# Kernel optimization log

Measured on AMD Instinct MI355X. Metric: run time of the kernel, lower is better.

## Reference

```python
import jax, jax.numpy as jnp
import numpy as np

D_MODEL = 512
D_FF = 2048
D_K = 64
N_HEADS = 8
LN_EPS = 1e-5


def layer_norm(x, gamma, beta):
    mu = jnp.mean(x, axis=-1, keepdims=True)
    var = jnp.mean(jnp.square(x - mu), axis=-1, keepdims=True)
    return (x - mu) * jax.lax.rsqrt(var + LN_EPS) * gamma + beta


def setup_inputs() -> dict:
    key = jax.random.key(0)
    ks = jax.random.split(key, 8)
    B, S = 16, 1024
    s_in = 1.0 / np.sqrt(D_MODEL)
    s_ff = 1.0 / np.sqrt(D_FF)
    return {
        "x": jax.random.normal(ks[0], (B, S, D_MODEL), jnp.float32),
        # shared QKV projection (the module uses ONE linear for Q, K and V)
        "w_qkv": jax.random.uniform(ks[1], (D_MODEL, D_MODEL), jnp.float32, -s_in, s_in),
        "b_qkv": jnp.zeros((D_MODEL,), jnp.float32),
        "w_out": jax.random.uniform(ks[2], (D_MODEL, D_MODEL), jnp.float32, -s_in, s_in),
        "b_out": jnp.zeros((D_MODEL,), jnp.float32),
        "w1": jax.random.uniform(ks[3], (D_FF, D_MODEL), jnp.float32, -s_in, s_in),
        "b1": jnp.zeros((D_FF,), jnp.float32),
        "w2": jax.random.uniform(ks[4], (D_MODEL, D_FF), jnp.float32, -s_ff, s_ff),
        "b2": jnp.zeros((D_MODEL,), jnp.float32),
        "g1": jnp.ones((D_MODEL,), jnp.float32),
        "be1": jnp.zeros((D_MODEL,), jnp.float32),
        "g2": jnp.ones((D_MODEL,), jnp.float32),
        "be2": jnp.zeros((D_MODEL,), jnp.float32),
    }


def reference(x, w_qkv, b_qkv, w_out, b_out, w1, b1, w2, b2, g1, be1, g2, be2):
    B, S, _ = x.shape
    # --- MultiHeadAttention (shared linear for Q/K/V, dropout = identity) ---
    qkv = x @ w_qkv.T + b_qkv                       # [B,S,D]
    h = qkv.reshape(B, S, N_HEADS, D_K)             # Q = K = V
    scores = jnp.einsum("bqhd,bkhd->bhqk", h, h) / np.sqrt(D_K)
    probs = jax.nn.softmax(scores, axis=-1)
    ctx = jnp.einsum("bhqk,bkhd->bqhd", probs, h).reshape(B, S, D_MODEL)
    attn = ctx @ w_out.T + b_out
    # --- dual-LayerNorm residual #1: x = norm1(x) + norm1(attn) ---
    x = layer_norm(x, g1, be1) + layer_norm(attn, g1, be1)
    # --- FFN ---
    ffn = jax.nn.relu(x @ w1.T + b1) @ w2.T + b2
    # --- residual #2: x = x + norm2(ffn) ---
    return x + layer_norm(ffn, g2, be2)
```

## Files before the change

### kernel.cpp

```cpp
#include <hip/hip_runtime.h>
#include <hip/hip_bf16.h>
#include <stdint.h>


using bf16 = __bf16;
typedef __attribute__((ext_vector_type(2))) __bf16 bf16x2;
typedef __attribute__((ext_vector_type(4))) __bf16 bf16x4;
typedef __attribute__((ext_vector_type(8))) __bf16 bf16x8;
typedef __attribute__((ext_vector_type(4))) float floatx4;
typedef __attribute__((ext_vector_type(16))) float f32x16;

#define AS1 __attribute__((address_space(1)))
#define AS3 __attribute__((address_space(3)))

#define L2E 1.44269504088896340736f

constexpr int BN_ = 16, SQ_ = 1024, DM_ = 512, DFF_ = 2048, NH_ = 8, DK_ = 64;
constexpr int ROWS_ = BN_ * SQ_;

__global__ __launch_bounds__(256) void f2b_kernel(const float* __restrict__ in,
                                                  bf16* __restrict__ out, int n8) {
  int i = blockIdx.x * 256 + threadIdx.x;
  if (i >= n8) return;
  float4 a = ((const float4*)in)[2 * i];
  float4 b = ((const float4*)in)[2 * i + 1];
  bf16x8 o;
  o[0] = (bf16)a.x; o[1] = (bf16)a.y; o[2] = (bf16)a.z; o[3] = (bf16)a.w;
  o[4] = (bf16)b.x; o[5] = (bf16)b.y; o[6] = (bf16)b.z; o[7] = (bf16)b.w;
  ((bf16x8*)out)[i] = o;
}

template <int RELU>
__global__ __launch_bounds__(256) void gemm_bt(const bf16* __restrict__ A,
                                               const bf16* __restrict__ B,
                                               const float* __restrict__ bias,
                                               bf16* __restrict__ C,
                                               int M, int N, int K) {
  __shared__ char glds[32768];
  const int tid = threadIdx.x;
  const int lane = tid & 63;
  const int wv = tid >> 6;
  const int wr = wv >> 1, wc = wv & 1;
  const int r15 = lane & 15, g = lane >> 4;
  const int tileN = blockIdx.x * 128;
  const int tileM = blockIdx.y * 128;

  floatx4 acc[4][4] = {};

  uint32_t dstoff[2];
  const bf16* srcA[2];
  const bf16* srcB[2];
#pragma unroll
  for (int is = 0; is < 2; ++is) {
    const int base = wv * 2048 + is * 1024;
    const int ob = base + lane * 16;
    const int row = ob >> 6;
    const int pslot = (ob >> 4) & 3;
    const int sslot = pslot ^ ((row >> 1) & 3);
    dstoff[is] = base;
    srcA[is] = A + (size_t)(tileM + row) * K + sslot * 8;
    srcB[is] = B + (size_t)(tileN + row) * K + sslot * 8;
  }

#define GSTAGE(buf, kt)                                                         \
  {                                                                             \
    _Pragma("unroll")                                                           \
    for (int is = 0; is < 2; ++is) {                                            \
      __builtin_amdgcn_global_load_lds(                                         \
          (AS1 uint32_t*)(srcA[is] + (kt) * 32),                                \
          (AS3 uint32_t*)((AS3 char*)glds + (buf) * 8192 + dstoff[is]), 16, 0, 0); \
      __builtin_amdgcn_global_load_lds(                                         \
          (AS1 uint32_t*)(srcB[is] + (kt) * 32),                                \
          (AS3 uint32_t*)((AS3 char*)glds + 16384 + (buf) * 8192 + dstoff[is]), \
          16, 0, 0);                                                            \
    }                                                                           \
  }

  uint32_t aoff[4], boff[4];
#pragma unroll
  for (int m = 0; m < 4; ++m) {
    const int arow = wr * 64 + m * 16 + r15;
    aoff[m] = (uint32_t)((arow * 64 + g * 16) ^ (((arow >> 1) & 3) << 4));
  }
#pragma unroll
  for (int n = 0; n < 4; ++n) {
    const int brow = wc * 64 + n * 16 + r15;
    boff[n] = (uint32_t)((brow * 64 + g * 16) ^ (((brow >> 1) & 3) << 4));
  }

  const int nk = K >> 5;
  GSTAGE(0, 0);

  for (int kt = 0; kt < nk; ++kt) {
    const int cur = kt & 1;
    if (kt + 1 < nk) {
      GSTAGE(cur ^ 1, kt + 1);
      asm volatile("s_waitcnt vmcnt(4)" ::: "memory");
    } else {
      asm volatile("s_waitcnt vmcnt(0)" ::: "memory");
    }
    __builtin_amdgcn_s_barrier();
    __builtin_amdgcn_sched_barrier(0);

    const char* Ac = (const char*)glds + cur * 8192;
    const char* Bc = (const char*)glds + 16384 + cur * 8192;

    bf16x8 af[4], bfr[4];
#pragma unroll
    for (int m = 0; m < 4; ++m) af[m] = *(const bf16x8*)(Ac + aoff[m]);
#pragma unroll
    for (int n = 0; n < 4; ++n) bfr[n] = *(const bf16x8*)(Bc + boff[n]);
#pragma unroll
    for (int m = 0; m < 4; ++m)
#pragma unroll
      for (int n = 0; n < 4; ++n)
        acc[m][n] = __builtin_amdgcn_mfma_f32_16x16x32_bf16(af[m], bfr[n],
                                                            acc[m][n], 0, 0, 0);
    __builtin_amdgcn_s_barrier();
  }
#undef GSTAGE

#pragma unroll
  for (int n = 0; n < 4; ++n) {
    const int col = tileN + wc * 64 + n * 16 + r15;
    const float bv = bias[col];
#pragma unroll
    for (int m = 0; m < 4; ++m) {
      const int row0 = tileM + wr * 64 + m * 16 + g * 4;
#pragma unroll
      for (int j = 0; j < 4; ++j) {
        float v = acc[m][n][j] + bv;
        if (RELU) v = fmaxf(v, 0.f);
        C[(size_t)(row0 + j) * N + col] = (bf16)v;
      }
    }
  }
}

__global__ __launch_bounds__(256) void attn_kernel(const bf16* __restrict__ qkv,
                                                   bf16* __restrict__ ctx) {
  __shared__ char lds[16384];

  const int tid = threadIdx.x;
  const int lane = tid & 63;
  const int wv = tid >> 6;
  const int l31 = lane & 31;
  const int h = lane >> 5;
  const int b = blockIdx.z, hd = blockIdx.y, qt = blockIdx.x;
  const size_t headoff = (size_t)b * SQ_ * DM_ + hd * DK_;
  const int q0 = qt * 128 + wv * 32;

  const float QS = 0.125f * L2E;
  bf16x8 aq[4];
#pragma unroll
  for (int kd = 0; kd < 4; ++kd) {
    const bf16* gq = qkv + headoff + (size_t)(q0 + l31) * DM_ + kd * 16 + h * 8;
    bf16x8 v = *(const bf16x8*)gq;
#pragma unroll
    for (int e = 0; e < 8; ++e) v[e] = (bf16)((float)v[e] * QS);
    aq[kd] = v;
  }

  f32x16 o0 = {}, o1 = {};
  float mstate = -1e30f, lstate = 0.f;

  const uint32_t ldsb = (uint32_t)(uintptr_t)(AS3 char*)lds;

  uint32_t dstoff[2];
  const bf16* srcb[2];
#pragma unroll
  for (int is = 0; is < 2; ++is) {
    const int ob = is * 4096 + wv * 1024 + lane * 16;
    const int e0 = ob >> 1;
    const int srow = ((e0 >> 8) << 2) + ((e0 >> 4) & 3);
    const int dcol = ((e0 >> 6) & 3) * 16 + ((e0 >> 3) & 1) * 8;
    dstoff[is] = is * 4096 + wv * 1024;
    srcb[is] = qkv + headoff + (size_t)srow * DM_ + dcol;
  }

#define STAGE(buf, t)                                                          \
  {                                                                            \
    _Pragma("unroll")                                                          \
    for (int is = 0; is < 2; ++is) {                                           \
      __builtin_amdgcn_global_load_lds(                                        \
          (AS1 uint32_t*)(srcb[is] + (size_t)(t) * 64 * DM_),                  \
          (AS3 uint32_t*)((AS3 char*)lds + (buf) * 8192 + dstoff[is]), 16, 0, 0); \
    }                                                                          \
  }

  constexpr int NT = SQ_ / 64;
  STAGE(0, 0);

  for (int t = 0; t < NT; ++t) {
    const int cur = t & 1;
    __builtin_amdgcn_s_barrier();
    if (t + 1 < NT) {
      STAGE(cur ^ 1, t + 1);
      asm volatile("s_waitcnt vmcnt(2)" ::: "memory");
    } else {
      asm volatile("s_waitcnt vmcnt(0)" ::: "memory");
    }
    __builtin_amdgcn_s_barrier();
    __builtin_amdgcn_sched_barrier(0);

    const char* tile = (const char*)lds + cur * 8192;

    f32x16 s0v = {}, s1v = {};
    const char* pabase = tile + (l31 >> 2) * 512 + (l31 & 3) * 32 + h * 16;
    __builtin_amdgcn_s_setprio(1);
#pragma unroll
    for (int kd = 0; kd < 4; ++kd) {
      bf16x8 a0 = *(const bf16x8*)(pabase + kd * 128);
      bf16x8 a1 = *(const bf16x8*)(pabase + kd * 128 + 4096);
      s0v = __builtin_amdgcn_mfma_f32_32x32x16_bf16(a0, aq[kd], s0v, 0, 0, 0);
      s1v = __builtin_amdgcn_mfma_f32_32x32x16_bf16(a1, aq[kd], s1v, 0, 0, 0);
    }
    __builtin_amdgcn_s_setprio(0);

    float mx = s0v[0];
#pragma unroll
    for (int r = 1; r < 16; ++r) mx = fmaxf(mx, s0v[r]);
#pragma unroll
    for (int r = 0; r < 16; ++r) mx = fmaxf(mx, s1v[r]);
    mx = fmaxf(mx, __shfl_xor(mx, 32));
    if (!__all(mx - mstate <= 8.f)) {
      const float nm = fmaxf(mstate, mx);
      const float al = exp2f(mstate - nm);
      mstate = nm;
      lstate *= al;
#pragma unroll
      for (int r = 0; r < 16; ++r) { o0[r] *= al; o1[r] *= al; }
    }
    float rs = 0.f;
#pragma unroll
    for (int r = 0; r < 16; ++r) {
      float p = exp2f(s0v[r] - mstate);
      s0v[r] = p; rs += p;
    }
#pragma unroll
    for (int r = 0; r < 16; ++r) {
      float p = exp2f(s1v[r] - mstate);
      s1v[r] = p; rs += p;
    }
    rs += __shfl_xor(rs, 32);
    lstate += rs;

    uint32_t pf[4][4];
#pragma unroll
    for (int ks = 0; ks < 4; ++ks) {
      const int kb = (ks & 1) * 8;
      float v0, v1, v2, v3, v4, v5, v6, v7;
      if (ks < 2) {
        v0 = s0v[kb+0]; v1 = s0v[kb+1]; v2 = s0v[kb+2]; v3 = s0v[kb+3];
        v4 = s0v[kb+4]; v5 = s0v[kb+5]; v6 = s0v[kb+6]; v7 = s0v[kb+7];
      } else {
        v0 = s1v[kb+0]; v1 = s1v[kb+1]; v2 = s1v[kb+2]; v3 = s1v[kb+3];
        v4 = s1v[kb+4]; v5 = s1v[kb+5]; v6 = s1v[kb+6]; v7 = s1v[kb+7];
      }
      union { bf16x2 v; uint32_t u; } P0, P1, P2, P3;
      P0.v = bf16x2{(bf16)v0, (bf16)v1};
      P1.v = bf16x2{(bf16)v2, (bf16)v3};
      P2.v = bf16x2{(bf16)v4, (bf16)v5};
      P3.v = bf16x2{(bf16)v6, (bf16)v7};
      asm volatile("v_permlane32_swap_b32 %0, %1" : "+v"(P0.u), "+v"(P2.u));
      asm volatile("v_permlane32_swap_b32 %0, %1" : "+v"(P1.u), "+v"(P3.u));
      pf[ks][0] = P0.u;
      pf[ks][1] = P1.u;
      pf[ks][2] = P2.u;
      pf[ks][3] = P3.u;
    }

#pragma unroll
    for (int df = 0; df < 2; ++df) {
      const uint32_t vb = ldsb + cur * 8192 + df * 256 + (lane & 15) * 8 +
                          ((lane >> 4) & 1) * 128 + (lane >> 5) * 1024;
      bf16x4 lo[4], hi[4];
#pragma unroll
      for (int ks = 0; ks < 4; ++ks) {
        asm volatile("ds_read_b64_tr_b16 %0, %2\n\t"
                     "ds_read_b64_tr_b16 %1, %2 offset:512"
                     : "=&v"(lo[ks]), "=&v"(hi[ks])
                     : "v"(vb + ks * 2048));
      }
      asm volatile("s_waitcnt lgkmcnt(0)" ::: "memory");
      __builtin_amdgcn_sched_barrier(0);
      __builtin_amdgcn_s_setprio(1);
#pragma unroll
      for (int ks = 0; ks < 4; ++ks) {
        union { struct { bf16x4 l, h; } p; bf16x8 v; } av;
        av.p.l = lo[ks]; av.p.h = hi[ks];
        union { uint32_t u[4]; bf16x8 v; } bv;
        bv.u[0] = pf[ks][0]; bv.u[1] = pf[ks][1];
        bv.u[2] = pf[ks][2]; bv.u[3] = pf[ks][3];
        if (df == 0)
          o0 = __builtin_amdgcn_mfma_f32_32x32x16_bf16(av.v, bv.v, o0, 0, 0, 0);
        else
          o1 = __builtin_amdgcn_mfma_f32_32x32x16_bf16(av.v, bv.v, o1, 0, 0, 0);
      }
      __builtin_amdgcn_s_setprio(0);
    }
  }
#undef STAGE

  __syncthreads();
  const float invl = 1.f / lstate;
  char* wb = (char*)lds + wv * 4096;
#pragma unroll
  for (int df = 0; df < 2; ++df)
#pragma unroll
    for (int t = 0; t < 4; ++t) {
      const f32x16& ov = df ? o1 : o0;
      bf16x4 pkt;
      pkt[0] = (bf16)(ov[4*t+0] * invl);
      pkt[1] = (bf16)(ov[4*t+1] * invl);
      pkt[2] = (bf16)(ov[4*t+2] * invl);
      pkt[3] = (bf16)(ov[4*t+3] * invl);
      const int byte = (l31 * 128 + df * 64 + t * 16 + h * 8) ^ ((l31 & 7) << 4);
      *(bf16x4*)(wb + byte) = pkt;
    }
#pragma unroll
  for (int ps = 0; ps < 4; ++ps) {
    const int qr = ps * 8 + (lane >> 3);
    const int byte = (qr * 128 + (lane & 7) * 16) ^ ((qr & 7) << 4);
    bf16x8 vv = *(const bf16x8*)(wb + byte);
    bf16* dst = ctx + (size_t)(b * SQ_ + q0 + qr) * DM_ + hd * 64 + (lane & 7) * 8;
    *(bf16x8*)dst = vv;
  }
}

__global__ __launch_bounds__(256) void dual_ln_kernel(const float* __restrict__ x,
                                                      const bf16* __restrict__ attn,
                                                      const float* __restrict__ g1,
                                                      const float* __restrict__ be1,
                                                      bf16* __restrict__ out) {
  const int row = blockIdx.x * 4 + (threadIdx.x >> 6);
  const int lane = threadIdx.x & 63;
  const float* xr = x + (size_t)row * DM_ + lane * 8;
  float xs[8], as_[8];
  float4 t0 = ((const float4*)xr)[0];
  float4 t1 = ((const float4*)xr)[1];
  xs[0] = t0.x; xs[1] = t0.y; xs[2] = t0.z; xs[3] = t0.w;
  xs[4] = t1.x; xs[5] = t1.y; xs[6] = t1.z; xs[7] = t1.w;
  bf16x8 av = *(const bf16x8*)(attn + (size_t)row * DM_ + lane * 8);
#pragma unroll
  for (int e = 0; e < 8; ++e) as_[e] = (float)av[e];
  float sx = 0, sx2 = 0, sa = 0, sa2 = 0;
#pragma unroll
  for (int e = 0; e < 8; ++e) {
    sx += xs[e]; sx2 += xs[e] * xs[e];
    sa += as_[e]; sa2 += as_[e] * as_[e];
  }
#pragma unroll
  for (int off = 1; off < 64; off <<= 1) {
    sx += __shfl_xor(sx, off);  sx2 += __shfl_xor(sx2, off);
    sa += __shfl_xor(sa, off);  sa2 += __shfl_xor(sa2, off);
  }
  const float inv = 1.f / (float)DM_;
  const float mux = sx * inv, mua = sa * inv;
  const float rx = rsqrtf(fmaxf(sx2 * inv - mux * mux, 0.f) + 1e-5f);
  const float ra = rsqrtf(fmaxf(sa2 * inv - mua * mua, 0.f) + 1e-5f);
  bf16x8 ov;
#pragma unroll
  for (int e = 0; e < 8; ++e) {
    const int c = lane * 8 + e;
    const float val = ((xs[e] - mux) * rx + (as_[e] - mua) * ra) * g1[c] + 2.f * be1[c];
    ov[e] = (bf16)val;
  }
  *(bf16x8*)(out + (size_t)row * DM_ + lane * 8) = ov;
}

__global__ __launch_bounds__(256) void final_ln_kernel(const bf16* __restrict__ x1,
                                                       const bf16* __restrict__ ffn,
                                                       const float* __restrict__ g2,
                                                       const float* __restrict__ be2,
                                                       float* __restrict__ out) {
  const int row = blockIdx.x * 4 + (threadIdx.x >> 6);
  const int lane = threadIdx.x & 63;
  bf16x8 xv = *(const bf16x8*)(x1 + (size_t)row * DM_ + lane * 8);
  bf16x8 fv = *(const bf16x8*)(ffn + (size_t)row * DM_ + lane * 8);
  float fs[8];
#pragma unroll
  for (int e = 0; e < 8; ++e) fs[e] = (float)fv[e];
  float sf = 0, sf2 = 0;
#pragma unroll
  for (int e = 0; e < 8; ++e) { sf += fs[e]; sf2 += fs[e] * fs[e]; }
#pragma unroll
  for (int off = 1; off < 64; off <<= 1) {
    sf += __shfl_xor(sf, off);  sf2 += __shfl_xor(sf2, off);
  }
  const float inv = 1.f / (float)DM_;
  const float mu = sf * inv;
  const float rs = rsqrtf(fmaxf(sf2 * inv - mu * mu, 0.f) + 1e-5f);
  float ov[8];
#pragma unroll
  for (int e = 0; e < 8; ++e) {
    const int c = lane * 8 + e;
    ov[e] = (float)xv[e] + (fs[e] - mu) * rs * g2[c] + be2[c];
  }
  float* orow = out + (size_t)row * DM_ + lane * 8;
  float4 o0 = {ov[0], ov[1], ov[2], ov[3]};
  float4 o1 = {ov[4], ov[5], ov[6], ov[7]};
  ((float4*)orow)[0] = o0;
  ((float4*)orow)[1] = o1;
}

extern "C" void kernel_launch(void* const* d_in, const int* in_sizes, int n_in,
                              void* d_out, int out_size, void* d_ws, size_t ws_size,
                              hipStream_t stream) {
  const float* x     = (const float*)d_in[0];
  const float* w_qkv = (const float*)d_in[1];
  const float* b_qkv = (const float*)d_in[2];
  const float* w_out = (const float*)d_in[3];
  const float* b_out = (const float*)d_in[4];
  const float* w1    = (const float*)d_in[5];
  const float* b1    = (const float*)d_in[6];
  const float* w2    = (const float*)d_in[7];
  const float* b2    = (const float*)d_in[8];
  const float* g1    = (const float*)d_in[9];
  const float* be1   = (const float*)d_in[10];
  const float* g2    = (const float*)d_in[11];
  const float* be2   = (const float*)d_in[12];
  float* out = (float*)d_out;

  char* ws = (char*)d_ws;
  const size_t o_wqkv = 0;
  const size_t o_wout = o_wqkv + (size_t)DM_ * DM_ * 2;
  const size_t o_w1   = o_wout + (size_t)DM_ * DM_ * 2;
  const size_t o_w2   = o_w1 + (size_t)DFF_ * DM_ * 2;
  const size_t o_A    = o_w2 + (size_t)DM_ * DFF_ * 2;
  const size_t o_B    = o_A + (size_t)ROWS_ * DM_ * 2;
  const size_t o_C    = o_B + (size_t)ROWS_ * DM_ * 2;
  const size_t o_D    = o_C + (size_t)ROWS_ * DM_ * 2;
  const size_t need   = o_D + (size_t)ROWS_ * DFF_ * 2;
  if (ws_size < need) return;

  bf16* wqkv_bf = (bf16*)(ws + o_wqkv);
  bf16* wout_bf = (bf16*)(ws + o_wout);
  bf16* w1_bf   = (bf16*)(ws + o_w1);
  bf16* w2_bf   = (bf16*)(ws + o_w2);
  bf16* bufA    = (bf16*)(ws + o_A);
  bf16* bufB    = (bf16*)(ws + o_B);
  bf16* bufC    = (bf16*)(ws + o_C);
  bf16* bufD    = (bf16*)(ws + o_D);

  f2b_kernel<<<dim3((ROWS_ * DM_ / 8 + 255) / 256), dim3(256), 0, stream>>>(x, bufA, ROWS_ * DM_ / 8);
  f2b_kernel<<<dim3((DM_ * DM_ / 8 + 255) / 256), dim3(256), 0, stream>>>(w_qkv, wqkv_bf, DM_ * DM_ / 8);
  f2b_kernel<<<dim3((DM_ * DM_ / 8 + 255) / 256), dim3(256), 0, stream>>>(w_out, wout_bf, DM_ * DM_ / 8);
  f2b_kernel<<<dim3((DFF_ * DM_ / 8 + 255) / 256), dim3(256), 0, stream>>>(w1, w1_bf, DFF_ * DM_ / 8);
  f2b_kernel<<<dim3((DM_ * DFF_ / 8 + 255) / 256), dim3(256), 0, stream>>>(w2, w2_bf, DM_ * DFF_ / 8);

  gemm_bt<0><<<dim3(DM_ / 128, ROWS_ / 128), dim3(256), 0, stream>>>(bufA, wqkv_bf, b_qkv, bufB, ROWS_, DM_, DM_);

  attn_kernel<<<dim3(SQ_ / 128, NH_, BN_), dim3(256), 0, stream>>>(bufB, bufA);

  gemm_bt<0><<<dim3(DM_ / 128, ROWS_ / 128), dim3(256), 0, stream>>>(bufA, wout_bf, b_out, bufC, ROWS_, DM_, DM_);

  dual_ln_kernel<<<dim3(ROWS_ / 4), dim3(256), 0, stream>>>(x, bufC, g1, be1, bufB);

  gemm_bt<1><<<dim3(DFF_ / 128, ROWS_ / 128), dim3(256), 0, stream>>>(bufB, w1_bf, b1, bufD, ROWS_, DFF_, DM_);

  gemm_bt<0><<<dim3(DM_ / 128, ROWS_ / 128), dim3(256), 0, stream>>>(bufD, w2_bf, b2, bufC, ROWS_, DM_, DFF_);

  final_ln_kernel<<<dim3(ROWS_ / 4), dim3(256), 0, stream>>>(bufB, bufC, g2, be2, out);
}
```

Measured before the change: 238.5 us.

## Enlarge GEMM M-tile to 256 and read bf16 x in dual LayerNorm

```diff
diff --git a/kernel.cpp b/kernel.cpp
--- a/kernel.cpp
+++ b/kernel.cpp
@@ -36,50 +36,62 @@
                                                const float* __restrict__ bias,
                                                bf16* __restrict__ C,
                                                int M, int N, int K) {
-  __shared__ char glds[32768];
+  __shared__ char glds[49152];
   const int tid = threadIdx.x;
   const int lane = tid & 63;
   const int wv = tid >> 6;
   const int wr = wv >> 1, wc = wv & 1;
   const int r15 = lane & 15, g = lane >> 4;
   const int tileN = blockIdx.x * 128;
-  const int tileM = blockIdx.y * 128;
-
-  floatx4 acc[4][4] = {};
-
-  uint32_t dstoff[2];
-  const bf16* srcA[2];
+  const int tileM = blockIdx.y * 256;
+
+  floatx4 acc[8][4] = {};
+
+  uint32_t dstoffA[4], dstoffB[2];
+  const bf16* srcA[4];
   const bf16* srcB[2];
 #pragma unroll
-  for (int is = 0; is < 2; ++is) {
-    const int base = wv * 2048 + is * 1024;
+  for (int is = 0; is < 4; ++is) {
+    const int base = is * 4096 + wv * 1024;
     const int ob = base + lane * 16;
     const int row = ob >> 6;
     const int pslot = (ob >> 4) & 3;
     const int sslot = pslot ^ ((row >> 1) & 3);
-    dstoff[is] = base;
+    dstoffA[is] = base;
     srcA[is] = A + (size_t)(tileM + row) * K + sslot * 8;
+  }
+#pragma unroll
+  for (int is = 0; is < 2; ++is) {
+    const int base = is * 4096 + wv * 1024;
+    const int ob = base + lane * 16;
+    const int row = ob >> 6;
+    const int pslot = (ob >> 4) & 3;
+    const int sslot = pslot ^ ((row >> 1) & 3);
+    dstoffB[is] = base;
     srcB[is] = B + (size_t)(tileN + row) * K + sslot * 8;
   }
 
-#define GSTAGE(buf, kt)                                                         \
-  {                                                                             \
-    _Pragma("unroll")                                                           \
-    for (int is = 0; is < 2; ++is) {                                            \
-      __builtin_amdgcn_global_load_lds(                                         \
-          (AS1 uint32_t*)(srcA[is] + (kt) * 32),                                \
-          (AS3 uint32_t*)((AS3 char*)glds + (buf) * 8192 + dstoff[is]), 16, 0, 0); \
-      __builtin_amdgcn_global_load_lds(                                         \
-          (AS1 uint32_t*)(srcB[is] + (kt) * 32),                                \
-          (AS3 uint32_t*)((AS3 char*)glds + 16384 + (buf) * 8192 + dstoff[is]), \
-          16, 0, 0);                                                            \
-    }                                                                           \
-  }
-
-  uint32_t aoff[4], boff[4];
-#pragma unroll
-  for (int m = 0; m < 4; ++m) {
-    const int arow = wr * 64 + m * 16 + r15;
+#define GSTAGE(buf, kt)                                                          \
+  {                                                                              \
+    _Pragma("unroll")                                                            \
+    for (int is = 0; is < 4; ++is) {                                             \
+      __builtin_amdgcn_global_load_lds(                                          \
+          (AS1 uint32_t*)(srcA[is] + (kt) * 32),                                 \
+          (AS3 uint32_t*)((AS3 char*)glds + (buf) * 16384 + dstoffA[is]), 16, 0, 0); \
+    }                                                                            \
+    _Pragma("unroll")                                                            \
+    for (int is = 0; is < 2; ++is) {                                             \
+      __builtin_amdgcn_global_load_lds(                                          \
+          (AS1 uint32_t*)(srcB[is] + (kt) * 32),                                 \
+          (AS3 uint32_t*)((AS3 char*)glds + 32768 + (buf) * 8192 + dstoffB[is]), \
+          16, 0, 0);                                                             \
+    }                                                                            \
+  }
+
+  uint32_t aoff[8], boff[4];
+#pragma unroll
+  for (int m = 0; m < 8; ++m) {
+    const int arow = wr * 128 + m * 16 + r15;
     aoff[m] = (uint32_t)((arow * 64 + g * 16) ^ (((arow >> 1) & 3) << 4));
   }
 #pragma unroll
@@ -95,23 +107,23 @@
     const int cur = kt & 1;
     if (kt + 1 < nk) {
       GSTAGE(cur ^ 1, kt + 1);
-      asm volatile("s_waitcnt vmcnt(4)" ::: "memory");
+      asm volatile("s_waitcnt vmcnt(6)" ::: "memory");
     } else {
       asm volatile("s_waitcnt vmcnt(0)" ::: "memory");
     }
     __builtin_amdgcn_s_barrier();
     __builtin_amdgcn_sched_barrier(0);
 
-    const char* Ac = (const char*)glds + cur * 8192;
-    const char* Bc = (const char*)glds + 16384 + cur * 8192;
-
-    bf16x8 af[4], bfr[4];
-#pragma unroll
-    for (int m = 0; m < 4; ++m) af[m] = *(const bf16x8*)(Ac + aoff[m]);
+    const char* Ac = (const char*)glds + cur * 16384;
+    const char* Bc = (const char*)glds + 32768 + cur * 8192;
+
+    bf16x8 af[8], bfr[4];
+#pragma unroll
+    for (int m = 0; m < 8; ++m) af[m] = *(const bf16x8*)(Ac + aoff[m]);
 #pragma unroll
     for (int n = 0; n < 4; ++n) bfr[n] = *(const bf16x8*)(Bc + boff[n]);
 #pragma unroll
-    for (int m = 0; m < 4; ++m)
+    for (int m = 0; m < 8; ++m)
 #pragma unroll
       for (int n = 0; n < 4; ++n)
         acc[m][n] = __builtin_amdgcn_mfma_f32_16x16x32_bf16(af[m], bfr[n],
@@ -125,8 +137,8 @@
     const int col = tileN + wc * 64 + n * 16 + r15;
     const float bv = bias[col];
 #pragma unroll
-    for (int m = 0; m < 4; ++m) {
-      const int row0 = tileM + wr * 64 + m * 16 + g * 4;
+    for (int m = 0; m < 8; ++m) {
+      const int row0 = tileM + wr * 128 + m * 16 + g * 4;
 #pragma unroll
       for (int j = 0; j < 4; ++j) {
         float v = acc[m][n][j] + bv;
@@ -328,22 +340,18 @@
   }
 }
 
-__global__ __launch_bounds__(256) void dual_ln_kernel(const float* __restrict__ x,
+__global__ __launch_bounds__(256) void dual_ln_kernel(const bf16* __restrict__ x,
                                                       const bf16* __restrict__ attn,
                                                       const float* __restrict__ g1,
                                                       const float* __restrict__ be1,
                                                       bf16* __restrict__ out) {
   const int row = blockIdx.x * 4 + (threadIdx.x >> 6);
   const int lane = threadIdx.x & 63;
-  const float* xr = x + (size_t)row * DM_ + lane * 8;
+  bf16x8 xv = *(const bf16x8*)(x + (size_t)row * DM_ + lane * 8);
+  bf16x8 av = *(const bf16x8*)(attn + (size_t)row * DM_ + lane * 8);
   float xs[8], as_[8];
-  float4 t0 = ((const float4*)xr)[0];
-  float4 t1 = ((const float4*)xr)[1];
-  xs[0] = t0.x; xs[1] = t0.y; xs[2] = t0.z; xs[3] = t0.w;
-  xs[4] = t1.x; xs[5] = t1.y; xs[6] = t1.z; xs[7] = t1.w;
-  bf16x8 av = *(const bf16x8*)(attn + (size_t)row * DM_ + lane * 8);
-#pragma unroll
-  for (int e = 0; e < 8; ++e) as_[e] = (float)av[e];
+#pragma unroll
+  for (int e = 0; e < 8; ++e) { xs[e] = (float)xv[e]; as_[e] = (float)av[e]; }
   float sx = 0, sx2 = 0, sa = 0, sa2 = 0;
 #pragma unroll
   for (int e = 0; e < 8; ++e) {
@@ -443,23 +451,23 @@
   bf16* bufC    = (bf16*)(ws + o_C);
   bf16* bufD    = (bf16*)(ws + o_D);
 
-  f2b_kernel<<<dim3((ROWS_ * DM_ / 8 + 255) / 256), dim3(256), 0, stream>>>(x, bufA, ROWS_ * DM_ / 8);
+  f2b_kernel<<<dim3((ROWS_ * DM_ / 8 + 255) / 256), dim3(256), 0, stream>>>(x, bufD, ROWS_ * DM_ / 8);
   f2b_kernel<<<dim3((DM_ * DM_ / 8 + 255) / 256), dim3(256), 0, stream>>>(w_qkv, wqkv_bf, DM_ * DM_ / 8);
   f2b_kernel<<<dim3((DM_ * DM_ / 8 + 255) / 256), dim3(256), 0, stream>>>(w_out, wout_bf, DM_ * DM_ / 8);
   f2b_kernel<<<dim3((DFF_ * DM_ / 8 + 255) / 256), dim3(256), 0, stream>>>(w1, w1_bf, DFF_ * DM_ / 8);
   f2b_kernel<<<dim3((DM_ * DFF_ / 8 + 255) / 256), dim3(256), 0, stream>>>(w2, w2_bf, DM_ * DFF_ / 8);
 
-  gemm_bt<0><<<dim3(DM_ / 128, ROWS_ / 128), dim3(256), 0, stream>>>(bufA, wqkv_bf, b_qkv, bufB, ROWS_, DM_, DM_);
+  gemm_bt<0><<<dim3(DM_ / 128, ROWS_ / 256), dim3(256), 0, stream>>>(bufD, wqkv_bf, b_qkv, bufB, ROWS_, DM_, DM_);
 
   attn_kernel<<<dim3(SQ_ / 128, NH_, BN_), dim3(256), 0, stream>>>(bufB, bufA);
 
-  gemm_bt<0><<<dim3(DM_ / 128, ROWS_ / 128), dim3(256), 0, stream>>>(bufA, wout_bf, b_out, bufC, ROWS_, DM_, DM_);
-
-  dual_ln_kernel<<<dim3(ROWS_ / 4), dim3(256), 0, stream>>>(x, bufC, g1, be1, bufB);
-
-  gemm_bt<1><<<dim3(DFF_ / 128, ROWS_ / 128), dim3(256), 0, stream>>>(bufB, w1_bf, b1, bufD, ROWS_, DFF_, DM_);
-
-  gemm_bt<0><<<dim3(DM_ / 128, ROWS_ / 128), dim3(256), 0, stream>>>(bufD, w2_bf, b2, bufC, ROWS_, DM_, DFF_);
+  gemm_bt<0><<<dim3(DM_ / 128, ROWS_ / 256), dim3(256), 0, stream>>>(bufA, wout_bf, b_out, bufC, ROWS_, DM_, DM_);
+
+  dual_ln_kernel<<<dim3(ROWS_ / 4), dim3(256), 0, stream>>>(bufD, bufC, g1, be1, bufB);
+
+  gemm_bt<1><<<dim3(DFF_ / 128, ROWS_ / 256), dim3(256), 0, stream>>>(bufB, w1_bf, b1, bufD, ROWS_, DFF_, DM_);
+
+  gemm_bt<0><<<dim3(DM_ / 128, ROWS_ / 256), dim3(256), 0, stream>>>(bufD, w2_bf, b2, bufC, ROWS_, DM_, DFF_);
 
   final_ln_kernel<<<dim3(ROWS_ / 4), dim3(256), 0, stream>>>(bufB, bufC, g2, be2, out);
 }
```

Measured after the change: 260.0 us. 9.0% more time.
